# Kernel tuning notes

Hardware: AMD Instinct MI355X
Metric: run time of the kernel (lower is better)

The kernel has to match this reference:

```python
import math
import jax, jax.numpy as jnp
import numpy as np

B, H, L = 8, 512, 4096
N = 64 // 2  # d_state//2 complex pairs
DT_MIN, DT_MAX = 1e-3, 0.1


def setup_inputs() -> dict:
    key = jax.random.key(0)
    k_u, k_dt, k_C, k_D, k_W = jax.random.split(key, 5)
    u = jax.random.normal(k_u, (B, H, L), dtype=jnp.float32)
    log_dt = jax.random.uniform(k_dt, (H,), dtype=jnp.float32) * (
        math.log(DT_MAX) - math.log(DT_MIN)) + math.log(DT_MIN)
    log_A_real = jnp.log(0.5 * jnp.ones((H, N), dtype=jnp.float32))
    A_imag = math.pi * jnp.broadcast_to(jnp.arange(N, dtype=jnp.float32), (H, N))
    C = jax.random.normal(k_C, (H, N, 2), dtype=jnp.float32)  # view_as_real of cfloat
    D = jax.random.normal(k_D, (H,), dtype=jnp.float32)
    W_out = jax.random.normal(k_W, (2 * H, H), dtype=jnp.float32) * 0.05  # 1x1 conv weight
    b_out = jnp.zeros((2 * H,), dtype=jnp.float32)
    return {"u": u, "log_dt": log_dt, "log_A_real": log_A_real, "A_imag": A_imag,
            "C": C, "D": D, "W_out": W_out, "b_out": b_out}


def _ssm_kernel(log_dt, log_A_real, A_imag, C, length):
    dt = jnp.exp(log_dt)                             # (H,)
    A = -jnp.exp(log_A_real) + 1j * A_imag           # (H,N) complex
    dtA = A * dt[:, None]                            # (H,N)
    l = jnp.arange(length, dtype=jnp.float32)
    K = jnp.exp(dtA[:, :, None] * l)                 # (H,N,L) complex Vandermonde
    Cc = C[..., 0] + 1j * C[..., 1]                  # (H,N)
    Cs = Cc * (jnp.exp(dtA) - 1.0) / A               # (H,N)
    return 2.0 * jnp.einsum('hn,hnl->hl', Cs, K).real  # (H,L) real kernel


def reference(u, log_dt, log_A_real, A_imag, C, D, W_out, b_out):
    length = u.shape[-1]
    k = _ssm_kernel(log_dt, log_A_real, A_imag, C, length)  # (H,L)
    n_fft = 2 * length
    k_f = jnp.fft.rfft(k, n=n_fft)                   # (H, L+1)
    u_f = jnp.fft.rfft(u, n=n_fft)                   # (B,H,L+1)
    y = jnp.fft.irfft(u_f * k_f, n=n_fft)[..., :length]  # FFT convolution
    y = y + u * D[:, None]                           # D skip connection
    y = jax.nn.gelu(y, approximate=False)            # torch nn.GELU = exact erf
    y = jnp.einsum('oh,bhl->bol', W_out, y) + b_out[:, None]  # 1x1 conv
    a, b = jnp.split(y, 2, axis=-2)                  # GLU over channel dim
    return a * jax.nn.sigmoid(b)
```

## Files before the change

### kernel.cpp

```cpp
#include <hip/hip_runtime.h>
#include <math.h>

constexpr int cB = 8, cH = 512, cL = 4096, cN = 32;
constexpr int cG = 32, cLC = 128;
constexpr int cHN = cH * cN;

constexpr size_t OF_RR  = 0;
constexpr size_t OF_RI  = (size_t)cHN;
constexpr size_t OF_RPR = (size_t)2*cHN;
constexpr size_t OF_RPI = (size_t)3*cHN;
constexpr size_t OF_C2R = (size_t)4*cHN;
constexpr size_t OF_C2I = (size_t)5*cHN;
constexpr size_t OF_DR  = (size_t)6*cHN;
constexpr size_t OF_DI  = (size_t)7*cHN;
constexpr size_t OF_K   = (size_t)8*cHN;
constexpr size_t OF_WP  = OF_K + (size_t)512*128;
constexpr size_t OF_A   = OF_WP + (size_t)1024*512/2;
constexpr size_t OF_V   = OF_A + (size_t)512*128*192/2;
constexpr size_t OF_XP  = OF_V + (size_t)512*64*128/2;
constexpr size_t OF_G   = OF_XP + (size_t)512*256*64/2;
constexpr size_t OF_GT  = OF_A;

typedef __bf16 bf16x8 __attribute__((ext_vector_type(8)));
typedef float  f32x4  __attribute__((ext_vector_type(4)));

static __device__ __forceinline__ ushort f2bf(float x) {
    unsigned u = __float_as_uint(x);
    unsigned r = (u + 0x7fffu + ((u >> 16) & 1u)) >> 16;
    return (ushort)r;
}
static __device__ __forceinline__ float bf2f(ushort v) {
    return __uint_as_float(((unsigned)v) << 16);
}
static __device__ __forceinline__ unsigned pk2(float a, float b) {
    return (unsigned)f2bf(a) | ((unsigned)f2bf(b) << 16);
}
static __device__ __forceinline__ float gelu(float v) {
    return 0.5f * v * (1.0f + erff(v * 0.70710678118654752f));
}
static __device__ __forceinline__ void gload16(const void* g, void* l) {
    __builtin_amdgcn_global_load_lds(
        (const __attribute__((address_space(1))) unsigned*)g,
        (__attribute__((address_space(3))) unsigned*)l, 16, 0, 0);
}

__global__ void k_consts(const float* __restrict__ log_dt,
                         const float* __restrict__ log_A_real,
                         const float* __restrict__ A_imag,
                         const float* __restrict__ Cin,
                         float* __restrict__ ws)
{
    int tid = blockIdx.x * 256 + threadIdx.x;
    if (tid >= cHN) return;
    int h = tid >> 5;
    float dt = expf(log_dt[h]);
    float Ar = -expf(log_A_real[tid]);
    float Ai = A_imag[tid];
    float dr = dt * Ar, di = dt * Ai;
    float er = expf(dr);
    float rr = er * cosf(di), ri = er * sinf(di);
    float erL = expf(dr * (float)cLC);
    float diL = di * (float)cLC;
    float rpr = erL * cosf(diL), rpi = erL * sinf(diL);
    float cr = Cin[2*tid], ci = Cin[2*tid+1];
    float nr = rr - 1.0f, ni = ri;
    float inv = 1.0f / (Ar*Ar + Ai*Ai);
    float wr = (nr*Ar + ni*Ai) * inv;
    float wi = (ni*Ar - nr*Ai) * inv;
    float csr = cr*wr - ci*wi;
    float csi = cr*wi + ci*wr;
    ws[OF_RR  + tid] = rr;  ws[OF_RI  + tid] = ri;
    ws[OF_RPR + tid] = rpr; ws[OF_RPI + tid] = rpi;
    ws[OF_C2R + tid] = 2.0f*csr; ws[OF_C2I + tid] = 2.0f*csi;
    ws[OF_DR  + tid] = dr;  ws[OF_DI  + tid] = di;
}

__global__ void k_pack_w(const float* __restrict__ W, ushort* __restrict__ Wp)
{
    int idx = blockIdx.x * 256 + threadIdx.x;
    int base = idx * 4;
    int m = base >> 9;
    int k = base & 511;
    int src = (m & 1) ? (512 + (m >> 1)) : (m >> 1);
    float4 v = *(const float4*)&W[(size_t)src * 512 + k];
    ushort4 o;
    o.x = f2bf(v.x); o.y = f2bf(v.y); o.z = f2bf(v.z); o.w = f2bf(v.w);
    *(ushort4*)&Wp[base] = o;
}

__global__ void k_vmat(const float* __restrict__ ws, ushort* __restrict__ wsu)
{
    int tid = blockIdx.x * 256 + threadIdx.x;
    int h = tid >> 5, n = tid & 31;
    float dr = ws[OF_DR + tid], di = ws[OF_DI + tid];
    float e127 = expf(dr * 127.f), a127 = di * 127.f;
    float pr = e127 * cosf(a127), pi_ = e127 * sinf(a127);
    float rie = expf(-dr);
    float rc = rie * cosf(di), rs = -rie * sinf(di);
    ushort* vre = wsu + 2*OF_V + ((size_t)h*64 + n) * 128;
    ushort* vim = wsu + 2*OF_V + ((size_t)h*64 + 32 + n) * 128;
    for (int j4 = 0; j4 < 128; j4 += 4) {
        ushort4 r4, i4;
        #pragma unroll
        for (int e = 0; e < 4; ++e) {
            ((ushort*)&r4)[e] = f2bf(pr);
            ((ushort*)&i4)[e] = f2bf(pi_);
            float npr = pr*rc - pi_*rs;
            float npi = pr*rs + pi_*rc;
            pr = npr; pi_ = npi;
        }
        *(ushort4*)&vre[j4] = r4;
        *(ushort4*)&vim[j4] = i4;
    }
}

__global__ void k_emat(const float* __restrict__ ws, float* __restrict__ wsf,
                       ushort* __restrict__ wsu)
{
    int tid = blockIdx.x * 256 + threadIdx.x;
    int h = tid >> 7, l = tid & 127;
    float fl = (float)l, fl1 = (float)(l + 1);
    const float* dr_ = ws + OF_DR + (size_t)h*32;
    const float* di_ = ws + OF_DI + (size_t)h*32;
    const float* c2r_ = ws + OF_C2R + (size_t)h*32;
    const float* c2i_ = ws + OF_C2I + (size_t)h*32;
    ushort* rowA = wsu + 2*OF_A + ((size_t)h*128 + l) * 192;
    float kacc = 0.f;
    for (int n4 = 0; n4 < 32; n4 += 4) {
        ushort4 prq, npq;
        #pragma unroll
        for (int e = 0; e < 4; ++e) {
            int n = n4 + e;
            float dr = dr_[n], di = di_[n], c2r = c2r_[n], c2i = c2i_[n];
            float e0 = expf(dr * fl), a0 = di * fl;
            float c0 = cosf(a0), s0 = sinf(a0);
            kacc += e0 * (c2r*c0 - c2i*s0);
            float e1 = expf(dr * fl1), a1 = di * fl1;
            float c1 = cosf(a1), s1 = sinf(a1);
            ((ushort*)&prq)[e] = f2bf(e1 * (c2r*c1 - c2i*s1));
            ((ushort*)&npq)[e] = f2bf(-e1 * (c2r*s1 + c2i*c1));
        }
        *(ushort4*)&rowA[128 + n4] = prq;
        *(ushort4*)&rowA[160 + n4] = npq;
    }
    wsf[OF_K + (size_t)h*128 + l] = kacc;
}

__global__ void k_build_T(const float* __restrict__ wsf, const float* __restrict__ Dvec,
                          ushort* __restrict__ wsu)
{
    __shared__ float kv[256];
    int t = threadIdx.x;
    int tid = blockIdx.x * 256 + t;
    int h = tid >> 7, l = tid & 127;
    kv[t] = wsf[OF_K + (size_t)blockIdx.x * 256 + t];
    __syncthreads();
    const float* krow = kv + ((t >> 7) << 7);
    float Dh = Dvec[h];
    ushort* row = wsu + 2*OF_A + ((size_t)h*128 + l) * 192;
    for (int j8 = 0; j8 < 128; j8 += 8) {
        uint4 q;
        unsigned w[4];
        #pragma unroll
        for (int p = 0; p < 4; ++p) {
            int j0 = j8 + 2*p, j1 = j0 + 1;
            float v0 = (j0 <= l) ? krow[l - j0] : 0.f;
            float v1 = (j1 <= l) ? krow[l - j1] : 0.f;
            if (j0 == l) v0 += Dh;
            if (j1 == l) v1 += Dh;
            w[p] = pk2(v0, v1);
        }
        q.x = w[0]; q.y = w[1]; q.z = w[2]; q.w = w[3];
        *(uint4*)&row[j8] = q;
    }
}

__global__ __launch_bounds__(256) void k_state_gemm(const float* __restrict__ u,
                                                    const ushort* __restrict__ wsu,
                                                    ushort* __restrict__ xp)
{
    __shared__ ushort Vs[64 * 136];
    __shared__ ushort Bs[256 * 40];
    const int t = threadIdx.x;
    const int h = blockIdx.x;
    const int wn = t >> 6, lane = t & 63;
    const int lm = lane & 15, q = lane >> 4;

    {
        int idx = t * 32;
        int row = idx >> 7, kk = idx & 127;
        const ushort* src = wsu + 2*OF_V + ((size_t)h*64 + row) * 128 + kk;
        uint4 v0 = *(const uint4*)&src[0],  v1 = *(const uint4*)&src[8];
        uint4 v2 = *(const uint4*)&src[16], v3 = *(const uint4*)&src[24];
        ushort* d = (ushort*)Vs + row * 136 + kk;
        *(uint4*)&d[0] = v0; *(uint4*)&d[8] = v1;
        *(uint4*)&d[16] = v2; *(uint4*)&d[24] = v3;
    }

    const int b = t >> 5, c = t & 31;
    f32x4 acc[4][4];
    #pragma unroll
    for (int i = 0; i < 4; ++i)
        #pragma unroll
        for (int j = 0; j < 4; ++j) acc[i][j] = (f32x4){0.f,0.f,0.f,0.f};

    for (int k0 = 0; k0 < 128; k0 += 32) {
        const float* up = u + ((size_t)(b*cH + h)) * cL + (size_t)c*128 + k0;
        float4 f[8];
        #pragma unroll
        for (int e = 0; e < 8; ++e) f[e] = *(const float4*)&up[4*e];
        __syncthreads();
        ushort* d = (ushort*)Bs + t * 40;
        #pragma unroll
        for (int e = 0; e < 4; ++e) {
            uint4 w;
            w.x = pk2(f[2*e].x, f[2*e].y);   w.y = pk2(f[2*e].z, f[2*e].w);
            w.z = pk2(f[2*e+1].x, f[2*e+1].y); w.w = pk2(f[2*e+1].z, f[2*e+1].w);
            *(uint4*)&d[8*e] = w;
        }
        __syncthreads();
        bf16x8 af[4], bfr[4];
        #pragma unroll
        for (int mi = 0; mi < 4; ++mi)
            af[mi] = *(const bf16x8*)&Vs[(16*mi + lm) * 136 + k0 + 8*q];
        #pragma unroll
        for (int ni = 0; ni < 4; ++ni)
            bfr[ni] = *(const bf16x8*)&Bs[(64*wn + 16*ni + lm) * 40 + 8*q];
        #pragma unroll
        for (int mi = 0; mi < 4; ++mi)
            #pragma unroll
            for (int ni = 0; ni < 4; ++ni)
                acc[mi][ni] = __builtin_amdgcn_mfma_f32_16x16x32_bf16(af[mi], bfr[ni], acc[mi][ni], 0,0,0);
    }
    #pragma unroll
    for (int mi = 0; mi < 4; ++mi)
        #pragma unroll
        for (int ni = 0; ni < 4; ++ni) {
            int col = 64*wn + 16*ni + lm;
            int comp = 16*mi + 4*q;
            ushort4 st;
            st.x = f2bf(acc[mi][ni][0]); st.y = f2bf(acc[mi][ni][1]);
            st.z = f2bf(acc[mi][ni][2]); st.w = f2bf(acc[mi][ni][3]);
            *(ushort4*)&xp[((size_t)h*256 + col) * 64 + comp] = st;
        }
}

__global__ __launch_bounds__(256) void k_scan2(const float* __restrict__ ws,
                                               ushort* __restrict__ xp)
{
    int tid = blockIdx.x * 256 + threadIdx.x;
    int n  = tid & 31;
    int bh = tid >> 5;
    int h  = bh & (cH - 1);
    int b  = bh >> 9;
    float rpr = ws[OF_RPR + (size_t)h*32 + n];
    float rpi = ws[OF_RPI + (size_t)h*32 + n];
    float Xr = 0.f, Xi = 0.f;
    ushort* base = xp + ((size_t)h*256 + (size_t)b*32) * 64 + n;
    for (int c = 0; c < cG; ++c) {
        ushort* p = base + (size_t)c * 64;
        float sr = bf2f(p[0]), si = bf2f(p[32]);
        p[0]  = f2bf(Xr);
        p[32] = f2bf(Xi);
        float nXr = fmaf(rpr, Xr, fmaf(-rpi, Xi, sr));
        float nXi = fmaf(rpr, Xi, fmaf(rpi, Xr, si));
        Xr = nXr; Xi = nXi;
    }
}

__global__ __launch_bounds__(256) void k_conv(const float* __restrict__ u,
                                              const ushort* __restrict__ wsu,
                                              ushort* __restrict__ g)
{
    __shared__ ushort As[128 * 40];
    __shared__ ushort Bs[128 * 40];
    const int t = threadIdx.x;
    const int ctile = blockIdx.x;
    const int h = blockIdx.y;
    const int wave = t >> 6, lane = t & 63;
    const int wm = wave & 1, wn = wave >> 1;
    const int lm = lane & 15, q = lane >> 4;

    const int arow = t & 127, ah = t >> 7;
    const int col = arow, half = ah;
    const int gc = ctile * 128 + col;
    const int ub = gc >> 5, uc = gc & 31;

    const ushort* Ab = wsu + 2*OF_A + ((size_t)h*128 + arow) * 192;
    const ushort* xpB = wsu + 2*OF_XP + ((size_t)h*256 + gc) * 64;

    f32x4 acc[4][4];
    #pragma unroll
    for (int i = 0; i < 4; ++i)
        #pragma unroll
        for (int j = 0; j < 4; ++j) acc[i][j] = (f32x4){0.f,0.f,0.f,0.f};

    for (int k0 = 0; k0 < 192; k0 += 32) {
        uint4 a0 = *(const uint4*)&Ab[k0 + 16*ah];
        uint4 a1 = *(const uint4*)&Ab[k0 + 16*ah + 8];
        uint4 b0, b1;
        if (k0 < 128) {
            const float* up = u + ((size_t)(ub*cH + h)) * cL + (size_t)uc*128 + k0 + 16*half;
            float4 f0 = *(const float4*)&up[0],  f1 = *(const float4*)&up[4];
            float4 f2 = *(const float4*)&up[8],  f3 = *(const float4*)&up[12];
            b0.x = pk2(f0.x,f0.y); b0.y = pk2(f0.z,f0.w);
            b0.z = pk2(f1.x,f1.y); b0.w = pk2(f1.z,f1.w);
            b1.x = pk2(f2.x,f2.y); b1.y = pk2(f2.z,f2.w);
            b1.z = pk2(f3.x,f3.y); b1.w = pk2(f3.z,f3.w);
        } else {
            const ushort* xs = xpB + (k0 - 128) + 16*half;
            b0 = *(const uint4*)&xs[0];
            b1 = *(const uint4*)&xs[8];
        }
        __syncthreads();
        *(uint4*)&As[arow*40 + 16*ah]     = a0;
        *(uint4*)&As[arow*40 + 16*ah + 8] = a1;
        *(uint4*)&Bs[col*40 + 16*half]     = b0;
        *(uint4*)&Bs[col*40 + 16*half + 8] = b1;
        __syncthreads();
        bool skip = (wm == 0) && (k0 == 64 || k0 == 96);
        if (!skip) {
            bf16x8 af[4], bfr[4];
            #pragma unroll
            for (int mi = 0; mi < 4; ++mi)
                af[mi] = *(const bf16x8*)&As[(64*wm + 16*mi + lm) * 40 + 8*q];
            #pragma unroll
            for (int ni = 0; ni < 4; ++ni)
                bfr[ni] = *(const bf16x8*)&Bs[(64*wn + 16*ni + lm) * 40 + 8*q];
            #pragma unroll
            for (int mi = 0; mi < 4; ++mi)
                #pragma unroll
                for (int ni = 0; ni < 4; ++ni)
                    acc[mi][ni] = __builtin_amdgcn_mfma_f32_16x16x32_bf16(af[mi], bfr[ni], acc[mi][ni], 0,0,0);
        }
    }
    #pragma unroll
    for (int ni = 0; ni < 4; ++ni) {
        int ocol = ctile*128 + 64*wn + 16*ni + lm;
        int ob = ocol >> 5, oc = ocol & 31;
        ushort* grow = g + ((size_t)(ob*cH + h)) * cL + (size_t)oc*128;
        #pragma unroll
        for (int mi = 0; mi < 4; ++mi) {
            int l = 64*wm + 16*mi + 4*q;
            ushort4 st;
            st.x = f2bf(gelu(acc[mi][ni][0]));
            st.y = f2bf(gelu(acc[mi][ni][1]));
            st.z = f2bf(gelu(acc[mi][ni][2]));
            st.w = f2bf(gelu(acc[mi][ni][3]));
            *(ushort4*)&grow[l] = st;
        }
    }
}

__global__ __launch_bounds__(256) void k_transpose(const ushort* __restrict__ gsrc,
                                                   ushort* __restrict__ gT)
{
    __shared__ ushort tile[64 * 64];
    const int t = threadIdx.x;
    const int b  = blockIdx.z;
    const int h0 = blockIdx.y << 6;
    const int l0 = blockIdx.x << 6;
    const ushort* gb = gsrc + ((size_t)b * cH + h0) * cL + l0;
    const int lb = t & 7;
    #pragma unroll
    for (int half = 0; half < 2; ++half) {
        int r = (t >> 3) + half * 32;
        uint4 v = *(const uint4*)&gb[(size_t)r * cL + lb * 8];
        int sb = lb ^ (r & 7) ^ (r >> 3);
        *(uint4*)&tile[r * 64 + sb * 8] = v;
    }
    __syncthreads();
    ushort* gTb = gT + ((size_t)b * cL + l0) * cH + h0;
    #pragma unroll
    for (int half = 0; half < 2; ++half) {
        int l  = (t >> 3) + half * 32;
        int hb = t & 7;
        ushort vals[8];
        #pragma unroll
        for (int e = 0; e < 8; ++e) {
            int r  = hb * 8 + e;
            int sb = (l >> 3) ^ (r & 7) ^ (r >> 3);
            vals[e] = tile[r * 64 + sb * 8 + (l & 7)];
        }
        *(uint4*)&gTb[(size_t)l * cH + hb * 8] = *(uint4*)vals;
    }
}

__global__ __launch_bounds__(256) void k_gemm2(const ushort* __restrict__ Wp,
                                               const float* __restrict__ bias,
                                               const ushort* __restrict__ gT,
                                               float* __restrict__ out)
{
    __shared__ ushort As[2][128 * 32];
    __shared__ ushort Bs[2][128 * 32];
    const int t    = threadIdx.x;
    const int l0   = blockIdx.x * 128;
    const int by   = blockIdx.y;
    const int b    = blockIdx.z;
    const int wave = t >> 6, lane = t & 63;
    const int wm   = wave & 1, wn = wave >> 1;
    const int lm   = lane & 15, q = lane >> 4;

    const int srow = lane >> 2;
    const int scol = (lane & 3) * 8;
    const ushort* Ag = Wp + (size_t)(by * 128) * 512;
    const ushort* Bg = gT + ((size_t)b * cL + l0) * 512;

    f32x4 acc[4][4];
    #pragma unroll
    for (int i = 0; i < 4; ++i)
        #pragma unroll
        for (int j = 0; j < 4; ++j)
            acc[i][j] = (f32x4){0.f, 0.f, 0.f, 0.f};

    auto stage = [&](ushort* Asb, ushort* Bsb, int k0) {
        #pragma unroll
        for (int j = 0; j < 2; ++j) {
            int row = 32*wave + 16*j + srow;
            gload16(Ag + (size_t)row * 512 + k0 + scol,
                    (char*)Asb + wave*2048 + j*1024);
            gload16(Bg + (size_t)row * 512 + k0 + scol,
                    (char*)Bsb + wave*2048 + j*1024);
        }
    };
    auto compute = [&](const ushort* Asb, const ushort* Bsb) {
        bf16x8 af[4], bfr[4];
        #pragma unroll
        for (int mi = 0; mi < 4; ++mi)
            af[mi] = *(const bf16x8*)&Asb[(64*wm + 16*mi + lm) * 32 + 8*q];
        #pragma unroll
        for (int ni = 0; ni < 4; ++ni)
            bfr[ni] = *(const bf16x8*)&Bsb[(64*wn + 16*ni + lm) * 32 + 8*q];
        #pragma unroll
        for (int mi = 0; mi < 4; ++mi)
            #pragma unroll
            for (int ni = 0; ni < 4; ++ni)
                acc[mi][ni] = __builtin_amdgcn_mfma_f32_16x16x32_bf16(af[mi], bfr[ni], acc[mi][ni], 0,0,0);
    };

    stage(As[0], Bs[0], 0);
    __syncthreads();
    int cur = 0;
    for (int ks = 0; ks < 15; ++ks) {
        stage(As[cur ^ 1], Bs[cur ^ 1], (ks + 1) * 32);
        compute(As[cur], Bs[cur]);
        __syncthreads();
        cur ^= 1;
    }
    compute(As[cur], Bs[cur]);

    const int obase = by * 64 + 32 * wm;
    #pragma unroll
    for (int mi = 0; mi < 4; ++mi) {
        #pragma unroll
        for (int p = 0; p < 2; ++p) {
            int o = obase + 8*mi + 2*q + p;
            float ba = bias[o], bb = bias[512 + o];
            float* orow = out + ((size_t)b * cH + o) * cL + l0 + 64*wn + lm;
            #pragma unroll
            for (int ni = 0; ni < 4; ++ni) {
                float av = acc[mi][ni][2*p]     + ba;
                float gv = acc[mi][ni][2*p + 1] + bb;
                orow[16 * ni] = av / (1.f + expf(-gv));
            }
        }
    }
}

extern "C" void kernel_launch(void* const* d_in, const int* in_sizes, int n_in,
                              void* d_out, int out_size, void* d_ws, size_t ws_size,
                              hipStream_t stream)
{
    (void)in_sizes; (void)n_in; (void)out_size; (void)ws_size;
    const float* u          = (const float*)d_in[0];
    const float* log_dt     = (const float*)d_in[1];
    const float* log_A_real = (const float*)d_in[2];
    const float* A_imag     = (const float*)d_in[3];
    const float* C          = (const float*)d_in[4];
    const float* D          = (const float*)d_in[5];
    const float* W          = (const float*)d_in[6];
    const float* bias       = (const float*)d_in[7];
    float* out = (float*)d_out;
    float* ws  = (float*)d_ws;
    ushort* wsu = (ushort*)d_ws;
    ushort* Wp  = wsu + 2*OF_WP;
    ushort* xp  = wsu + 2*OF_XP;
    ushort* gbf = wsu + 2*OF_G;
    ushort* gTu = wsu + 2*OF_GT;

    hipLaunchKernelGGL(k_consts, dim3(cHN/256), dim3(256), 0, stream,
                       log_dt, log_A_real, A_imag, C, ws);
    hipLaunchKernelGGL(k_pack_w, dim3(1024*512/4/256), dim3(256), 0, stream, W, Wp);
    hipLaunchKernelGGL(k_vmat, dim3(cHN/256), dim3(256), 0, stream, ws, wsu);
    hipLaunchKernelGGL(k_emat, dim3(512*128/256), dim3(256), 0, stream, ws, ws, wsu);
    hipLaunchKernelGGL(k_build_T, dim3(512*128/256), dim3(256), 0, stream, ws, D, wsu);
    hipLaunchKernelGGL(k_state_gemm, dim3(512), dim3(256), 0, stream, u, wsu, xp);
    hipLaunchKernelGGL(k_scan2, dim3(cB*cH*cN/256), dim3(256), 0, stream, ws, xp);
    hipLaunchKernelGGL(k_conv, dim3(2, 512), dim3(256), 0, stream, u, wsu, gbf);
    hipLaunchKernelGGL(k_transpose, dim3(cL/64, cH/64, cB), dim3(256), 0, stream, gbf, gTu);
    hipLaunchKernelGGL(k_gemm2, dim3(cL/128, 1024/128, cB), dim3(256), 0, stream,
                       Wp, bias, gTu, out);
}
```

Baseline: 290.9 us.

## Fuse setup kernels and stage full conv operands in LDS per head

Merges the constants kernel with the Vandermonde-matrix kernel, and the E-matrix kernel with the Toeplitz build, so the SSM kernel values pass through shared memory instead of a global round-trip. This removes two launches. The conv GEMM now runs one 512-thread block per head and loads the whole A tile (128x192) and B tile (256x192, u converted to bf16 plus scan states) into LDS once. That drops the per-k-step double barrier and global reloads. The cost is about 150KB of LDS per block, which limits occupancy to one block per CU, and load latency is no longer overlapped with MFMA work.

```diff
diff --git a/kernel.cpp b/kernel.cpp
--- a/kernel.cpp
+++ b/kernel.cpp
@@ -44,15 +44,16 @@
         (__attribute__((address_space(3))) unsigned*)l, 16, 0, 0);
 }
 
-__global__ void k_consts(const float* __restrict__ log_dt,
-                         const float* __restrict__ log_A_real,
-                         const float* __restrict__ A_imag,
-                         const float* __restrict__ Cin,
-                         float* __restrict__ ws)
+__global__ void k_consts_vmat(const float* __restrict__ log_dt,
+                              const float* __restrict__ log_A_real,
+                              const float* __restrict__ A_imag,
+                              const float* __restrict__ Cin,
+                              float* __restrict__ ws,
+                              ushort* __restrict__ wsu)
 {
     int tid = blockIdx.x * 256 + threadIdx.x;
     if (tid >= cHN) return;
-    int h = tid >> 5;
+    int h = tid >> 5, n = tid & 31;
     float dt = expf(log_dt[h]);
     float Ar = -expf(log_A_real[tid]);
     float Ai = A_imag[tid];
@@ -73,6 +74,26 @@
     ws[OF_RPR + tid] = rpr; ws[OF_RPI + tid] = rpi;
     ws[OF_C2R + tid] = 2.0f*csr; ws[OF_C2I + tid] = 2.0f*csi;
     ws[OF_DR  + tid] = dr;  ws[OF_DI  + tid] = di;
+
+    float e127 = expf(dr * 127.f), a127 = di * 127.f;
+    float pr = e127 * cosf(a127), pi_ = e127 * sinf(a127);
+    float rie = expf(-dr);
+    float rc = rie * cosf(di), rs = -rie * sinf(di);
+    ushort* vre = wsu + 2*OF_V + ((size_t)h*64 + n) * 128;
+    ushort* vim = wsu + 2*OF_V + ((size_t)h*64 + 32 + n) * 128;
+    for (int j4 = 0; j4 < 128; j4 += 4) {
+        ushort4 r4, i4;
+        #pragma unroll
+        for (int e = 0; e < 4; ++e) {
+            ((ushort*)&r4)[e] = f2bf(pr);
+            ((ushort*)&i4)[e] = f2bf(pi_);
+            float npr = pr*rc - pi_*rs;
+            float npi = pr*rs + pi_*rc;
+            pr = npr; pi_ = npi;
+        }
+        *(ushort4*)&vre[j4] = r4;
+        *(ushort4*)&vim[j4] = i4;
+    }
 }
 
 __global__ void k_pack_w(const float* __restrict__ W, ushort* __restrict__ Wp)
@@ -88,36 +109,12 @@
     *(ushort4*)&Wp[base] = o;
 }
 
-__global__ void k_vmat(const float* __restrict__ ws, ushort* __restrict__ wsu)
-{
-    int tid = blockIdx.x * 256 + threadIdx.x;
-    int h = tid >> 5, n = tid & 31;
-    float dr = ws[OF_DR + tid], di = ws[OF_DI + tid];
-    float e127 = expf(dr * 127.f), a127 = di * 127.f;
-    float pr = e127 * cosf(a127), pi_ = e127 * sinf(a127);
-    float rie = expf(-dr);
-    float rc = rie * cosf(di), rs = -rie * sinf(di);
-    ushort* vre = wsu + 2*OF_V + ((size_t)h*64 + n) * 128;
-    ushort* vim = wsu + 2*OF_V + ((size_t)h*64 + 32 + n) * 128;
-    for (int j4 = 0; j4 < 128; j4 += 4) {
-        ushort4 r4, i4;
-        #pragma unroll
-        for (int e = 0; e < 4; ++e) {
-            ((ushort*)&r4)[e] = f2bf(pr);
-            ((ushort*)&i4)[e] = f2bf(pi_);
-            float npr = pr*rc - pi_*rs;
-            float npi = pr*rs + pi_*rc;
-            pr = npr; pi_ = npi;
-        }
-        *(ushort4*)&vre[j4] = r4;
-        *(ushort4*)&vim[j4] = i4;
-    }
-}
-
-__global__ void k_emat(const float* __restrict__ ws, float* __restrict__ wsf,
+__global__ void k_embt(const float* __restrict__ ws, const float* __restrict__ Dvec,
                        ushort* __restrict__ wsu)
 {
-    int tid = blockIdx.x * 256 + threadIdx.x;
+    __shared__ float kv[256];
+    int t = threadIdx.x;
+    int tid = blockIdx.x * 256 + t;
     int h = tid >> 7, l = tid & 127;
     float fl = (float)l, fl1 = (float)(l + 1);
     const float* dr_ = ws + OF_DR + (size_t)h*32;
@@ -143,21 +140,10 @@
         *(ushort4*)&rowA[128 + n4] = prq;
         *(ushort4*)&rowA[160 + n4] = npq;
     }
-    wsf[OF_K + (size_t)h*128 + l] = kacc;
-}
-
-__global__ void k_build_T(const float* __restrict__ wsf, const float* __restrict__ Dvec,
-                          ushort* __restrict__ wsu)
-{
-    __shared__ float kv[256];
-    int t = threadIdx.x;
-    int tid = blockIdx.x * 256 + t;
-    int h = tid >> 7, l = tid & 127;
-    kv[t] = wsf[OF_K + (size_t)blockIdx.x * 256 + t];
+    kv[t] = kacc;
     __syncthreads();
     const float* krow = kv + ((t >> 7) << 7);
     float Dh = Dvec[h];
-    ushort* row = wsu + 2*OF_A + ((size_t)h*128 + l) * 192;
     for (int j8 = 0; j8 < 128; j8 += 8) {
         uint4 q;
         unsigned w[4];
@@ -171,7 +157,7 @@
             w[p] = pk2(v0, v1);
         }
         q.x = w[0]; q.y = w[1]; q.z = w[2]; q.w = w[3];
-        *(uint4*)&row[j8] = q;
+        *(uint4*)&rowA[j8] = q;
     }
 }
 
@@ -268,26 +254,47 @@
     }
 }
 
-__global__ __launch_bounds__(256) void k_conv(const float* __restrict__ u,
+__global__ __launch_bounds__(512) void k_conv(const float* __restrict__ u,
                                               const ushort* __restrict__ wsu,
                                               ushort* __restrict__ g)
 {
-    __shared__ ushort As[128 * 40];
-    __shared__ ushort Bs[128 * 40];
+    __shared__ ushort As[128 * 200];
+    __shared__ ushort Bs[256 * 200];
     const int t = threadIdx.x;
-    const int ctile = blockIdx.x;
-    const int h = blockIdx.y;
+    const int h = blockIdx.x;
     const int wave = t >> 6, lane = t & 63;
     const int wm = wave & 1, wn = wave >> 1;
     const int lm = lane & 15, q = lane >> 4;
 
-    const int arow = t & 127, ah = t >> 7;
-    const int col = arow, half = ah;
-    const int gc = ctile * 128 + col;
-    const int ub = gc >> 5, uc = gc & 31;
-
-    const ushort* Ab = wsu + 2*OF_A + ((size_t)h*128 + arow) * 192;
-    const ushort* xpB = wsu + 2*OF_XP + ((size_t)h*256 + gc) * 64;
+    {
+        const int row = t >> 2, c0 = (t & 3) * 48;
+        const ushort* Ab = wsu + 2*OF_A + ((size_t)h*128 + row) * 192 + c0;
+        ushort* d = &As[row * 200 + c0];
+        #pragma unroll
+        for (int e = 0; e < 6; ++e)
+            *(uint4*)&d[8*e] = *(const uint4*)&Ab[8*e];
+    }
+    {
+        const int gc = t >> 1, half = t & 1;
+        const int ub = gc >> 5, uc = gc & 31;
+        const float* up = u + ((size_t)(ub*cH + h)) * cL + (size_t)uc*128 + half*64;
+        ushort* d = &Bs[gc * 200 + half*64];
+        #pragma unroll
+        for (int e = 0; e < 8; ++e) {
+            float4 f0 = *(const float4*)&up[8*e];
+            float4 f1 = *(const float4*)&up[8*e + 4];
+            uint4 w;
+            w.x = pk2(f0.x, f0.y); w.y = pk2(f0.z, f0.w);
+            w.z = pk2(f1.x, f1.y); w.w = pk2(f1.z, f1.w);
+            *(uint4*)&d[8*e] = w;
+        }
+        const ushort* xs = wsu + 2*OF_XP + ((size_t)h*256 + gc) * 64 + half*32;
+        ushort* dx = &Bs[gc * 200 + 128 + half*32];
+        #pragma unroll
+        for (int e = 0; e < 4; ++e)
+            *(uint4*)&dx[8*e] = *(const uint4*)&xs[8*e];
+    }
+    __syncthreads();
 
     f32x4 acc[4][4];
     #pragma unroll
@@ -295,49 +302,26 @@
         #pragma unroll
         for (int j = 0; j < 4; ++j) acc[i][j] = (f32x4){0.f,0.f,0.f,0.f};
 
+    #pragma unroll
     for (int k0 = 0; k0 < 192; k0 += 32) {
-        uint4 a0 = *(const uint4*)&Ab[k0 + 16*ah];
-        uint4 a1 = *(const uint4*)&Ab[k0 + 16*ah + 8];
-        uint4 b0, b1;
-        if (k0 < 128) {
-            const float* up = u + ((size_t)(ub*cH + h)) * cL + (size_t)uc*128 + k0 + 16*half;
-            float4 f0 = *(const float4*)&up[0],  f1 = *(const float4*)&up[4];
-            float4 f2 = *(const float4*)&up[8],  f3 = *(const float4*)&up[12];
-            b0.x = pk2(f0.x,f0.y); b0.y = pk2(f0.z,f0.w);
-            b0.z = pk2(f1.x,f1.y); b0.w = pk2(f1.z,f1.w);
-            b1.x = pk2(f2.x,f2.y); b1.y = pk2(f2.z,f2.w);
-            b1.z = pk2(f3.x,f3.y); b1.w = pk2(f3.z,f3.w);
-        } else {
-            const ushort* xs = xpB + (k0 - 128) + 16*half;
-            b0 = *(const uint4*)&xs[0];
-            b1 = *(const uint4*)&xs[8];
-        }
-        __syncthreads();
-        *(uint4*)&As[arow*40 + 16*ah]     = a0;
-        *(uint4*)&As[arow*40 + 16*ah + 8] = a1;
-        *(uint4*)&Bs[col*40 + 16*half]     = b0;
-        *(uint4*)&Bs[col*40 + 16*half + 8] = b1;
-        __syncthreads();
-        bool skip = (wm == 0) && (k0 == 64 || k0 == 96);
-        if (!skip) {
-            bf16x8 af[4], bfr[4];
-            #pragma unroll
-            for (int mi = 0; mi < 4; ++mi)
-                af[mi] = *(const bf16x8*)&As[(64*wm + 16*mi + lm) * 40 + 8*q];
+        if ((wm == 0) && (k0 == 64 || k0 == 96)) continue;
+        bf16x8 af[4], bfr[4];
+        #pragma unroll
+        for (int mi = 0; mi < 4; ++mi)
+            af[mi] = *(const bf16x8*)&As[(64*wm + 16*mi + lm) * 200 + k0 + 8*q];
+        #pragma unroll
+        for (int ni = 0; ni < 4; ++ni)
+            bfr[ni] = *(const bf16x8*)&Bs[(64*wn + 16*ni + lm) * 200 + k0 + 8*q];
+        #pragma unroll
+        for (int mi = 0; mi < 4; ++mi)
             #pragma unroll
             for (int ni = 0; ni < 4; ++ni)
-                bfr[ni] = *(const bf16x8*)&Bs[(64*wn + 16*ni + lm) * 40 + 8*q];
-            #pragma unroll
-            for (int mi = 0; mi < 4; ++mi)
-                #pragma unroll
-                for (int ni = 0; ni < 4; ++ni)
-                    acc[mi][ni] = __builtin_amdgcn_mfma_f32_16x16x32_bf16(af[mi], bfr[ni], acc[mi][ni], 0,0,0);
-        }
+                acc[mi][ni] = __builtin_amdgcn_mfma_f32_16x16x32_bf16(af[mi], bfr[ni], acc[mi][ni], 0,0,0);
     }
     #pragma unroll
     for (int ni = 0; ni < 4; ++ni) {
-        int ocol = ctile*128 + 64*wn + 16*ni + lm;
-        int ob = ocol >> 5, oc = ocol & 31;
+        int gc = 64*wn + 16*ni + lm;
+        int ob = gc >> 5, oc = gc & 31;
         ushort* grow = g + ((size_t)(ob*cH + h)) * cL + (size_t)oc*128;
         #pragma unroll
         for (int mi = 0; mi < 4; ++mi) {
@@ -488,15 +472,13 @@
     ushort* gbf = wsu + 2*OF_G;
     ushort* gTu = wsu + 2*OF_GT;
 
-    hipLaunchKernelGGL(k_consts, dim3(cHN/256), dim3(256), 0, stream,
-                       log_dt, log_A_real, A_imag, C, ws);
+    hipLaunchKernelGGL(k_consts_vmat, dim3(cHN/256), dim3(256), 0, stream,
+                       log_dt, log_A_real, A_imag, C, ws, wsu);
     hipLaunchKernelGGL(k_pack_w, dim3(1024*512/4/256), dim3(256), 0, stream, W, Wp);
-    hipLaunchKernelGGL(k_vmat, dim3(cHN/256), dim3(256), 0, stream, ws, wsu);
-    hipLaunchKernelGGL(k_emat, dim3(512*128/256), dim3(256), 0, stream, ws, ws, wsu);
-    hipLaunchKernelGGL(k_build_T, dim3(512*128/256), dim3(256), 0, stream, ws, D, wsu);
+    hipLaunchKernelGGL(k_embt, dim3(512*128/256), dim3(256), 0, stream, ws, D, wsu);
     hipLaunchKernelGGL(k_state_gemm, dim3(512), dim3(256), 0, stream, u, wsu, xp);
     hipLaunchKernelGGL(k_scan2, dim3(cB*cH*cN/256), dim3(256), 0, stream, ws, xp);
-    hipLaunchKernelGGL(k_conv, dim3(2, 512), dim3(256), 0, stream, u, wsu, gbf);
+    hipLaunchKernelGGL(k_conv, dim3(512), dim3(512), 0, stream, u, wsu, gbf);
     hipLaunchKernelGGL(k_transpose, dim3(cL/64, cH/64, cB), dim3(256), 0, stream, gbf, gTu);
     hipLaunchKernelGGL(k_gemm2, dim3(cL/128, 1024/128, cB), dim3(256), 0, stream,
                        Wp, bias, gTu, out);
```

Measured after the change: 282.9 us. -2.7%, faster.
